# Optimization experiments

Hardware: AMD Instinct MI355X
Metric: run time of the kernel (lower is better)

Reference implementation:

```python
import jax, jax.numpy as jnp
import numpy as np

E = 2048   # embedding_size
H = 2048   # hidden_size
B = 512    # batch
OUT = 2    # output_size (coords)


def setup_inputs() -> dict:
    key = jax.random.key(0)
    ks = jax.random.split(key, 11)
    s = 0.02
    return {
        "embedding": jax.random.normal(ks[0], (B, E), dtype=jnp.float32),
        "max_seq_length": 256,
        "W_embed": jax.random.normal(ks[1], (H, E), dtype=jnp.float32) * s,
        "b_embed": jnp.zeros((H,), dtype=jnp.float32),
        "W_ih": jax.random.normal(ks[2], (4 * H, OUT), dtype=jnp.float32) * s,
        "b_ih": jnp.zeros((4 * H,), dtype=jnp.float32),
        "W_hh": jax.random.normal(ks[3], (4 * H, H), dtype=jnp.float32) * s,
        "b_hh": jnp.zeros((4 * H,), dtype=jnp.float32),
        "W_out": jax.random.normal(ks[4], (OUT, H), dtype=jnp.float32) * s,
        "b_out": jnp.zeros((OUT,), dtype=jnp.float32),
        "W_stop": jax.random.normal(ks[5], (1, H), dtype=jnp.float32) * s,
        "b_stop": jnp.zeros((1,), dtype=jnp.float32),
    }


def reference(embedding, max_seq_length, W_embed, b_embed, W_ih, b_ih,
              W_hh, b_hh, W_out, b_out, W_stop, b_stop):
    # h_0 from embedding head (num_layers == 1)
    h0 = embedding @ W_embed.T + b_embed          # (B, H)
    c0 = jnp.zeros_like(h0)
    x0 = jnp.zeros((embedding.shape[0], OUT), dtype=embedding.dtype)

    def step(carry, _):
        h, c, x = carry
        gates = x @ W_ih.T + b_ih + h @ W_hh.T + b_hh    # (B, 4H)
        i, f, g, o = jnp.split(gates, 4, axis=-1)         # torch gate order i,f,g,o
        c = jax.nn.sigmoid(f) * c + jax.nn.sigmoid(i) * jnp.tanh(g)
        h = jax.nn.sigmoid(o) * jnp.tanh(c)
        coord = h @ W_out.T + b_out                        # (B, 2)
        stop = jax.nn.sigmoid(h @ W_stop.T + b_stop)       # (B, 1)
        return (h, c, coord), (coord, stop)

    _, (coords, stops) = jax.lax.scan(step, (h0, c0, x0), xs=None,
                                      length=max_seq_length)
    outputs = jnp.transpose(coords, (1, 0, 2))     # (B, T, 2)
    stop_probs = jnp.transpose(stops, (1, 0, 2))   # (B, T, 1)
    return outputs, stop_probs
```

## Files before the change

kernel.cpp:

```cpp
#include <hip/hip_runtime.h>
#include <stdint.h>

#define E_DIM 2048
#define H_DIM 2048
#define B_DIM 512
#define T_DIM 256
#define G4H   8192

typedef unsigned short u16;
typedef __attribute__((ext_vector_type(8))) short bf16x8;
typedef __attribute__((ext_vector_type(4))) float f32x4;

__device__ inline u16 f2b(float f) {
  union { float f; uint32_t i; } v; v.f = f;
  uint32_t u = v.i;
  return (u16)((u + 0x7FFFu + ((u >> 16) & 1u)) >> 16);
}
__device__ inline float b2f(u16 u) {
  union { uint32_t i; float f; } v; v.i = ((uint32_t)u) << 16; return v.f;
}

__global__ __launch_bounds__(256) void convert_bf16(const float* __restrict__ s,
                                                    u16* __restrict__ d, int n4) {
  int i = blockIdx.x * 256 + threadIdx.x;
  if (i < n4) {
    float4 f = ((const float4*)s)[i];
    ushort4 o;
    o.x = f2b(f.x); o.y = f2b(f.y); o.z = f2b(f.z); o.w = f2b(f.w);
    ((ushort4*)d)[i] = o;
  }
}

__global__ __launch_bounds__(256) void build_weff(const float* __restrict__ W,
                                                  const float* __restrict__ W_ih,
                                                  const float* __restrict__ W_out,
                                                  u16* __restrict__ Wz) {
  int id = blockIdx.x * 256 + threadIdx.x;
  int lane = id & 63;
  int k32  = (id >> 6) & 63;
  int n16  = id >> 12;
  int np = n16 * 16 + (lane & 15);
  int k  = k32 * 32 + (lane >> 4) * 8;
  int g = np & 3, jrow = np >> 2;
  int src = g * H_DIM + jrow;
  float wi0 = W_ih[src * 2 + 0], wi1 = W_ih[src * 2 + 1];
  const float* sw = W + (size_t)src * H_DIM + k;
  u16 out[8];
  for (int j = 0; j < 8; ++j) {
    float v = sw[j] + wi0 * W_out[k + j] + wi1 * W_out[H_DIM + k + j];
    out[j] = f2b(v);
  }
  u16* dst = Wz + (size_t)id * 8;
  *(ushort4*)(dst) = *(ushort4*)&out[0];
  *(ushort4*)(dst + 4) = *(ushort4*)&out[4];
}

__global__ __launch_bounds__(256) void build_epi(const float* __restrict__ b_ih,
                                                 const float* __restrict__ b_hh,
                                                 const float* __restrict__ W_ih,
                                                 const float* __restrict__ b_out,
                                                 float* __restrict__ epi) {
  int np = blockIdx.x * 256 + threadIdx.x;
  int src = (np & 3) * H_DIM + (np >> 2);
  float wi0 = W_ih[src * 2 + 0], wi1 = W_ih[src * 2 + 1];
  float4 e;
  e.x = b_ih[src] + b_hh[src] + b_out[0] * wi0 + b_out[1] * wi1;
  e.y = wi0;
  e.z = wi1;
  e.w = 0.f;
  ((float4*)epi)[np] = e;
}

#define BM 64
#define BN 128
#define BK 32
__global__ __launch_bounds__(256) void gemm_bt(const u16* __restrict__ A,
                                               const u16* __restrict__ Bm,
                                               float* __restrict__ C,
                                               int M, int N, int K) {
  __shared__ u16 sA[BM * BK];
  __shared__ u16 sB[BN * BK];
  const int t = threadIdx.x;
  const int bm0 = blockIdx.y * BM, bn0 = blockIdx.x * BN;
  const int wave = t >> 6, lane = t & 63;
  const int wm = (wave >> 1) * 32, wn = (wave & 1) * 64;
  const int r16 = lane & 15, quad = lane >> 4;

  f32x4 acc[2][4];
  const f32x4 z = {0.f, 0.f, 0.f, 0.f};
  for (int i = 0; i < 2; ++i)
    for (int j = 0; j < 4; ++j) acc[i][j] = z;

  const int arow = t >> 2, acg = t & 3;

  for (int k0 = 0; k0 < K; k0 += BK) {
    __syncthreads();
    *(uint4*)&sA[arow * BK + acg * 8] =
        *(const uint4*)&A[(size_t)(bm0 + arow) * K + k0 + acg * 8];
    for (int i = 0; i < 2; ++i) {
      int c = t + 256 * i;
      int row = c >> 2, cg = c & 3;
      *(uint4*)&sB[row * BK + cg * 8] =
          *(const uint4*)&Bm[(size_t)(bn0 + row) * K + k0 + cg * 8];
    }
    __syncthreads();
    bf16x8 af[2], bfr[4];
    for (int mt = 0; mt < 2; ++mt)
      af[mt] = *(const bf16x8*)&sA[(wm + mt * 16 + r16) * BK + quad * 8];
    for (int nt = 0; nt < 4; ++nt)
      bfr[nt] = *(const bf16x8*)&sB[(wn + nt * 16 + r16) * BK + quad * 8];
    for (int mt = 0; mt < 2; ++mt)
      for (int nt = 0; nt < 4; ++nt)
        acc[mt][nt] = __builtin_amdgcn_mfma_f32_16x16x32_bf16(af[mt], bfr[nt],
                                                              acc[mt][nt], 0, 0, 0);
  }
  for (int mt = 0; mt < 2; ++mt)
    for (int nt = 0; nt < 4; ++nt) {
      int row = bm0 + wm + mt * 16 + quad * 4;
      int col = bn0 + wn + nt * 16 + r16;
      for (int r = 0; r < 4; ++r)
        C[(size_t)(row + r) * N + col] = acc[mt][nt][r];
    }
}

__global__ __launch_bounds__(256) void init_state(const float* __restrict__ h0pre,
                                                  const float* __restrict__ b_embed,
                                                  u16* __restrict__ h,
                                                  float* __restrict__ c,
                                                  float* __restrict__ xzero) {
  int idx = blockIdx.x * 256 + threadIdx.x;
  int bg = idx >> 11, k = idx & (H_DIM - 1);
  float v = h0pre[idx] + b_embed[k];
  size_t chunk = (((size_t)(bg >> 4)) * 64 + (k >> 5)) * 64 + ((k >> 3) & 3) * 16 + (bg & 15);
  size_t pos = chunk * 8 + (k & 7);
  h[pos] = f2b(v);
  c[pos] = 0.f;
  if (idx < B_DIM * 2) xzero[idx] = 0.f;
}

__global__ __launch_bounds__(64) void calc_xcorr(const float* __restrict__ h0pre,
                                                 const float* __restrict__ b_embed,
                                                 const float* __restrict__ W_out,
                                                 const float* __restrict__ b_out,
                                                 float* __restrict__ xc) {
  int m = blockIdx.x, ln = threadIdx.x;
  float s0 = 0.f, s1 = 0.f;
  for (int k = ln; k < H_DIM; k += 64) {
    float hv = h0pre[(size_t)m * H_DIM + k] + b_embed[k];
    s0 += hv * W_out[k];
    s1 += hv * W_out[H_DIM + k];
  }
  for (int off = 32; off > 0; off >>= 1) {
    s0 += __shfl_down(s0, off);
    s1 += __shfl_down(s1, off);
  }
  if (ln == 0) {
    xc[m * 2 + 0] = -(s0 + b_out[0]);
    xc[m * 2 + 1] = -(s1 + b_out[1]);
  }
}

__global__ __launch_bounds__(256) void init_out(const float* __restrict__ b_out,
                                                const float* __restrict__ b_stop,
                                                float* __restrict__ coords,
                                                float* __restrict__ stops) {
  int i = blockIdx.x * 256 + threadIdx.x;
  coords[i * 2 + 0] = b_out[0];
  coords[i * 2 + 1] = b_out[1];
  stops[i] = b_stop[0];
}

__global__ __launch_bounds__(256) void finalize_stops(float* __restrict__ stops) {
  int i = blockIdx.x * 256 + threadIdx.x;
  stops[i] = 1.f / (1.f + __expf(-stops[i]));
}

__global__ __launch_bounds__(512) void gemm_lstm(const u16* __restrict__ hA,
                                                 const u16* __restrict__ Wz,
                                                 const float* __restrict__ epi,
                                                 const float* __restrict__ x,
                                                 float* __restrict__ c,
                                                 u16* __restrict__ h_out,
                                                 const float* __restrict__ W_out,
                                                 const float* __restrict__ W_stop,
                                                 float* __restrict__ coords,
                                                 float* __restrict__ stops,
                                                 int trow) {
  __shared__ char smem[131072];
  float* cb = (float*)smem;
  float* gt = (float*)smem;

  const int bid = blockIdx.x;
  const int nt = (bid & 7) * 8 + ((bid >> 3) & 7);
  const int mt = bid >> 6;
  const int bm0 = mt * 128;

  const int t = threadIdx.x, wv = t >> 6, ln = t & 63;
  const int wn2 = wv & 1, kq = wv >> 1;
  const int r16 = ln & 15, quad = ln >> 4;

  const u16* pA[8];
  const u16* pB[4];
  for (int i = 0; i < 8; ++i)
    pA[i] = hA + (size_t)((bm0 >> 4) + i) * 32768 + (size_t)(kq * 16) * 512 + ln * 8;
  for (int i = 0; i < 4; ++i)
    pB[i] = Wz + (size_t)(nt * 8 + wn2 * 4 + i) * 32768 + (size_t)(kq * 16) * 512 + ln * 8;

  f32x4 acc[8][4];
  const f32x4 z = {0.f, 0.f, 0.f, 0.f};
  for (int i = 0; i < 8; ++i)
    for (int j = 0; j < 4; ++j) acc[i][j] = z;

  bf16x8 af[2][8], bf[2][4];
  for (int i = 0; i < 8; ++i) af[0][i] = *(const bf16x8*)(pA[i]);
  for (int i = 0; i < 4; ++i) bf[0][i] = *(const bf16x8*)(pB[i]);

#pragma unroll 2
  for (int kk = 0; kk < 16; ++kk) {
    const int cu = kk & 1;
    if (kk < 15) {
      const int nx = cu ^ 1;
      const size_t off = (size_t)(kk + 1) * 512;
      for (int i = 0; i < 8; ++i) af[nx][i] = *(const bf16x8*)(pA[i] + off);
      for (int i = 0; i < 4; ++i) bf[nx][i] = *(const bf16x8*)(pB[i] + off);
    }
    for (int mi = 0; mi < 8; ++mi)
      for (int ni = 0; ni < 4; ++ni)
        acc[mi][ni] = __builtin_amdgcn_mfma_f32_16x16x32_bf16(af[cu][mi], bf[cu][ni],
                                                              acc[mi][ni], 0, 0, 0);
  }

  if (kq >= 2) {
    float* dst = cb + ((kq - 2) * 2 + wn2) * 8192;
    for (int mi = 0; mi < 8; ++mi)
      for (int ni = 0; ni < 4; ++ni)
        *(f32x4*)&dst[((mi * 4 + ni) * 64 + ln) * 4] = acc[mi][ni];
  }
  __syncthreads();
  if (kq < 2) {
    const float* src = cb + (kq * 2 + wn2) * 8192;
    for (int mi = 0; mi < 8; ++mi)
      for (int ni = 0; ni < 4; ++ni)
        acc[mi][ni] += *(const f32x4*)&src[((mi * 4 + ni) * 64 + ln) * 4];
  }
  __syncthreads();
  if (kq == 1) {
    float* dst = cb + wn2 * 8192;
    for (int mi = 0; mi < 8; ++mi)
      for (int ni = 0; ni < 4; ++ni)
        *(f32x4*)&dst[((mi * 4 + ni) * 64 + ln) * 4] = acc[mi][ni];
  }
  __syncthreads();
  if (kq == 0) {
    const float* src = cb + wn2 * 8192;
    for (int mi = 0; mi < 8; ++mi)
      for (int ni = 0; ni < 4; ++ni)
        acc[mi][ni] += *(const f32x4*)&src[((mi * 4 + ni) * 64 + ln) * 4];
  }

  for (int half = 0; half < 2; ++half) {
    __syncthreads();
    if (wv < 2) {
      for (int mi = 0; mi < 4; ++mi)
        for (int ni = 0; ni < 4; ++ni) {
          int row = mi * 16 + quad * 4;
          int col = wn2 * 64 + ni * 16 + r16;
          f32x4 v = acc[half * 4 + mi][ni];
          for (int r = 0; r < 4; ++r)
            gt[(row + r) * 132 + col] = v[r];
        }
    }
    __syncthreads();
    if ((wv >> 2) == half) {
      const int q = wv & 3;
      const int lrow = q * 16 + r16;
      const int bg = bm0 + half * 64 + lrow;
      const float x0 = x[bg * 2 + 0], x1 = x[bg * 2 + 1];
      const size_t chunk = (((size_t)(bg >> 4)) * 64 + nt) * 64 + ln;
      const int hc0 = nt * 32 + quad * 8;
      float cv[8]; u16 hv[8];
      float s0 = 0.f, s1 = 0.f, s2 = 0.f;
      const float4* epi4 = (const float4*)epi;
      for (int j = 0; j < 8; ++j) {
        int col = quad * 32 + j * 4;
        float4 g4 = *(const float4*)&gt[lrow * 132 + col];
        float4 e0 = epi4[nt * 128 + col + 0];
        float4 e1 = epi4[nt * 128 + col + 1];
        float4 e2 = epi4[nt * 128 + col + 2];
        float4 e3 = epi4[nt * 128 + col + 3];
        float gi = g4.x + e0.x + x0 * e0.y + x1 * e0.z;
        float gf = g4.y + e1.x + x0 * e1.y + x1 * e1.z;
        float gg = g4.z + e2.x + x0 * e2.y + x1 * e2.z;
        float go = g4.w + e3.x + x0 * e3.y + x1 * e3.z;
        float si = 1.f / (1.f + __expf(-gi));
        float sf = 1.f / (1.f + __expf(-gf));
        float so = 1.f / (1.f + __expf(-go));
        float cn = sf * c[chunk * 8 + j] + si * tanhf(gg);
        cv[j] = cn;
        float hf = so * tanhf(cn);
        hv[j] = f2b(hf);
        s0 += hf * W_out[hc0 + j];
        s1 += hf * W_out[H_DIM + hc0 + j];
        s2 += hf * W_stop[hc0 + j];
      }
      *(float4*)&c[chunk * 8 + 0] = *(float4*)&cv[0];
      *(float4*)&c[chunk * 8 + 4] = *(float4*)&cv[4];
      *(ushort4*)&h_out[chunk * 8 + 0] = *(ushort4*)&hv[0];
      *(ushort4*)&h_out[chunk * 8 + 4] = *(ushort4*)&hv[4];
      s0 += __shfl_xor(s0, 16); s1 += __shfl_xor(s1, 16); s2 += __shfl_xor(s2, 16);
      s0 += __shfl_xor(s0, 32); s1 += __shfl_xor(s1, 32); s2 += __shfl_xor(s2, 32);
      if (quad == 0) {
        atomicAdd(&coords[((size_t)bg * T_DIM + trow) * 2 + 0], s0);
        atomicAdd(&coords[((size_t)bg * T_DIM + trow) * 2 + 1], s1);
        atomicAdd(&stops[(size_t)bg * T_DIM + trow], s2);
      }
    }
  }
}

extern "C" void kernel_launch(void* const* d_in, const int* in_sizes, int n_in,
                              void* d_out, int out_size, void* d_ws, size_t ws_size,
                              hipStream_t stream) {
  const float* embedding = (const float*)d_in[0];
  const float* W_embed   = (const float*)d_in[2];
  const float* b_embed   = (const float*)d_in[3];
  const float* W_ih      = (const float*)d_in[4];
  const float* b_ih      = (const float*)d_in[5];
  const float* W_hh      = (const float*)d_in[6];
  const float* b_hh      = (const float*)d_in[7];
  const float* W_out     = (const float*)d_in[8];
  const float* b_out     = (const float*)d_in[9];
  const float* W_stop    = (const float*)d_in[10];
  const float* b_stop    = (const float*)d_in[11];

  float* coords = (float*)d_out;
  float* stops  = (float*)d_out + (size_t)B_DIM * T_DIM * 2;

  char* ws = (char*)d_ws;
  u16* W_z     = (u16*)ws;   ws += (size_t)G4H * H_DIM * 2;
  u16* W_emb_b = (u16*)ws;   ws += (size_t)H_DIM * E_DIM * 2;
  u16* emb_b   = (u16*)ws;   ws += (size_t)B_DIM * E_DIM * 2;
  float* h0pre = (float*)ws; ws += (size_t)B_DIM * H_DIM * 4;
  float* epi   = (float*)ws; ws += (size_t)G4H * 4 * 4;
  float* cbuf  = (float*)ws; ws += (size_t)B_DIM * H_DIM * 4;
  u16* hbuf0   = (u16*)ws;   ws += (size_t)B_DIM * H_DIM * 2;
  u16* hbuf1   = (u16*)ws;   ws += (size_t)B_DIM * H_DIM * 2;
  float* xcorr = (float*)ws; ws += (size_t)B_DIM * 2 * 4;
  float* xzero = (float*)ws; ws += (size_t)B_DIM * 2 * 4;

  convert_bf16<<<(B_DIM * E_DIM / 4 + 255) / 256, 256, 0, stream>>>(embedding, emb_b, B_DIM * E_DIM / 4);
  convert_bf16<<<(H_DIM * E_DIM / 4 + 255) / 256, 256, 0, stream>>>(W_embed, W_emb_b, H_DIM * E_DIM / 4);
  build_weff<<<(G4H * H_DIM / 8) / 256, 256, 0, stream>>>(W_hh, W_ih, W_out, W_z);
  build_epi<<<G4H / 256, 256, 0, stream>>>(b_ih, b_hh, W_ih, b_out, epi);
  init_out<<<(B_DIM * T_DIM) / 256, 256, 0, stream>>>(b_out, b_stop, coords, stops);

  gemm_bt<<<dim3(H_DIM / BN, B_DIM / BM), 256, 0, stream>>>(emb_b, W_emb_b, h0pre,
                                                            B_DIM, H_DIM, E_DIM);
  init_state<<<(B_DIM * H_DIM) / 256, 256, 0, stream>>>(h0pre, b_embed, hbuf0, cbuf, xzero);
  calc_xcorr<<<B_DIM, 64, 0, stream>>>(h0pre, b_embed, W_out, b_out, xcorr);

  for (int t = 0; t < T_DIM; ++t) {
    u16* h_in  = (t & 1) ? hbuf1 : hbuf0;
    u16* h_out = (t & 1) ? hbuf0 : hbuf1;
    const float* xv = (t == 0) ? xcorr : xzero;
    gemm_lstm<<<256, 512, 0, stream>>>(h_in, W_z, epi, xv, cbuf, h_out,
                                       W_out, W_stop, coords, stops, t);
  }
  finalize_stops<<<(B_DIM * T_DIM) / 256, 256, 0, stream>>>(stops);
}
```

Baseline: 8.044 ms.

## Stage GEMM operand tiles into LDS via async global_load_lds with double buffering

Each step's LSTM GEMM previously had every wave load its A and B fragments straight from global memory into registers. Now the block cooperatively copies tiles into LDS with global_load_lds, double-buffered across K steps, and the waves then read fragments from LDS. The wave split changes from 4-way K partitioning to 2-way K by 2x2 M/N, which halves the per-wave accumulator and simplifies the cross-wave reduction and epilogue. The launch bounds now request 2 blocks per CU, but the 128KB LDS buffer may prevent that. A barrier is added on every K step.

```diff
diff --git a/kernel.cpp b/kernel.cpp
--- a/kernel.cpp
+++ b/kernel.cpp
@@ -18,6 +18,12 @@
 }
 __device__ inline float b2f(u16 u) {
   union { uint32_t i; float f; } v; v.i = ((uint32_t)u) << 16; return v.f;
+}
+
+__device__ __forceinline__ void stage16(const void* g, void* l) {
+  __builtin_amdgcn_global_load_lds(
+      (const __attribute__((address_space(1))) uint32_t*)g,
+      (__attribute__((address_space(3))) uint32_t*)l, 16, 0, 0);
 }
 
 __global__ __launch_bounds__(256) void convert_bf16(const float* __restrict__ s,
@@ -175,7 +181,7 @@
   stops[i] = 1.f / (1.f + __expf(-stops[i]));
 }
 
-__global__ __launch_bounds__(512) void gemm_lstm(const u16* __restrict__ hA,
+__global__ __launch_bounds__(512, 2) void gemm_lstm(const u16* __restrict__ hA,
                                                  const u16* __restrict__ Wz,
                                                  const float* __restrict__ epi,
                                                  const float* __restrict__ x,
@@ -186,9 +192,7 @@
                                                  float* __restrict__ coords,
                                                  float* __restrict__ stops,
                                                  int trow) {
-  __shared__ char smem[131072];
-  float* cb = (float*)smem;
-  float* gt = (float*)smem;
+  __shared__ __align__(16) char smem[131072];
 
   const int bid = blockIdx.x;
   const int nt = (bid & 7) * 8 + ((bid >> 3) & 7);
@@ -196,124 +200,150 @@
   const int bm0 = mt * 128;
 
   const int t = threadIdx.x, wv = t >> 6, ln = t & 63;
-  const int wn2 = wv & 1, kq = wv >> 1;
+  const int kq = wv >> 2, wm = (wv >> 1) & 1, wn = wv & 1;
   const int r16 = ln & 15, quad = ln >> 4;
 
-  const u16* pA[8];
-  const u16* pB[4];
-  for (int i = 0; i < 8; ++i)
-    pA[i] = hA + (size_t)((bm0 >> 4) + i) * 32768 + (size_t)(kq * 16) * 512 + ln * 8;
+  const u16* gptr[8];
+  uint32_t ldsoff[8];
+#pragma unroll
+  for (int s = 0; s < 8; ++s) {
+    int ti = wv * 8 + s;
+    int g = ti >> 4;
+    int w = ti & 15;
+    int rowi = w >> 1, kc2 = w & 1;
+    int kqg = g >> 1, isB = g & 1;
+    int kc = kqg * 32 + kc2;
+    if (isB)
+      gptr[s] = Wz + ((size_t)(nt * 8 + rowi) * 64 + kc) * 512 + ln * 8;
+    else
+      gptr[s] = hA + ((size_t)((bm0 >> 4) + rowi) * 64 + kc) * 512 + ln * 8;
+    ldsoff[s] = (uint32_t)(kqg * 65536 + isB * 16384 + w * 1024);
+  }
+
+#pragma unroll
+  for (int s = 0; s < 8; ++s) stage16(gptr[s], smem + ldsoff[s]);
+#pragma unroll
+  for (int s = 0; s < 8; ++s) gptr[s] += 1024;
+  __syncthreads();
+
+  f32x4 acc[4][4];
+  const f32x4 z = {0.f, 0.f, 0.f, 0.f};
+#pragma unroll
   for (int i = 0; i < 4; ++i)
-    pB[i] = Wz + (size_t)(nt * 8 + wn2 * 4 + i) * 32768 + (size_t)(kq * 16) * 512 + ln * 8;
-
-  f32x4 acc[8][4];
-  const f32x4 z = {0.f, 0.f, 0.f, 0.f};
-  for (int i = 0; i < 8; ++i)
+#pragma unroll
     for (int j = 0; j < 4; ++j) acc[i][j] = z;
 
-  bf16x8 af[2][8], bf[2][4];
-  for (int i = 0; i < 8; ++i) af[0][i] = *(const bf16x8*)(pA[i]);
-  for (int i = 0; i < 4; ++i) bf[0][i] = *(const bf16x8*)(pB[i]);
-
-#pragma unroll 2
-  for (int kk = 0; kk < 16; ++kk) {
-    const int cu = kk & 1;
-    if (kk < 15) {
-      const int nx = cu ^ 1;
-      const size_t off = (size_t)(kk + 1) * 512;
-      for (int i = 0; i < 8; ++i) af[nx][i] = *(const bf16x8*)(pA[i] + off);
-      for (int i = 0; i < 4; ++i) bf[nx][i] = *(const bf16x8*)(pB[i] + off);
-    }
-    for (int mi = 0; mi < 8; ++mi)
-      for (int ni = 0; ni < 4; ++ni)
-        acc[mi][ni] = __builtin_amdgcn_mfma_f32_16x16x32_bf16(af[cu][mi], bf[cu][ni],
-                                                              acc[mi][ni], 0, 0, 0);
-  }
-
-  if (kq >= 2) {
-    float* dst = cb + ((kq - 2) * 2 + wn2) * 8192;
-    for (int mi = 0; mi < 8; ++mi)
+  const uint32_t rdbase0 = (uint32_t)(kq * 65536);
+
+  for (int p = 0; p < 16; ++p) {
+    if (p < 15) {
+      const uint32_t tog = (uint32_t)(((p + 1) & 1) * 32768);
+#pragma unroll
+      for (int s = 0; s < 8; ++s) stage16(gptr[s], smem + (ldsoff[s] + tog));
+#pragma unroll
+      for (int s = 0; s < 8; ++s) gptr[s] += 1024;
+    }
+    const char* rb = smem + rdbase0 + (uint32_t)((p & 1) * 32768);
+#pragma unroll
+    for (int kc2 = 0; kc2 < 2; ++kc2) {
+      bf16x8 af[4], bf[4];
+#pragma unroll
+      for (int i = 0; i < 4; ++i)
+        af[i] = *(const bf16x8*)(rb + ((wm * 4 + i) * 2 + kc2) * 1024 + ln * 16);
+#pragma unroll
+      for (int i = 0; i < 4; ++i)
+        bf[i] = *(const bf16x8*)(rb + 16384 + ((wn * 4 + i) * 2 + kc2) * 1024 + ln * 16);
+#pragma unroll
+      for (int mi = 0; mi < 4; ++mi)
+#pragma unroll
+        for (int ni = 0; ni < 4; ++ni)
+          acc[mi][ni] = __builtin_amdgcn_mfma_f32_16x16x32_bf16(af[mi], bf[ni],
+                                                                acc[mi][ni], 0, 0, 0);
+    }
+    __syncthreads();
+  }
+
+  float* cb = (float*)smem;
+  if (kq == 1) {
+    float* dst = cb + (wm * 2 + wn) * 4096;
+#pragma unroll
+    for (int mi = 0; mi < 4; ++mi)
+#pragma unroll
       for (int ni = 0; ni < 4; ++ni)
         *(f32x4*)&dst[((mi * 4 + ni) * 64 + ln) * 4] = acc[mi][ni];
   }
   __syncthreads();
-  if (kq < 2) {
-    const float* src = cb + (kq * 2 + wn2) * 8192;
-    for (int mi = 0; mi < 8; ++mi)
+  if (kq == 0) {
+    const float* src = cb + (wm * 2 + wn) * 4096;
+#pragma unroll
+    for (int mi = 0; mi < 4; ++mi)
+#pragma unroll
       for (int ni = 0; ni < 4; ++ni)
         acc[mi][ni] += *(const f32x4*)&src[((mi * 4 + ni) * 64 + ln) * 4];
   }
   __syncthreads();
-  if (kq == 1) {
-    float* dst = cb + wn2 * 8192;
-    for (int mi = 0; mi < 8; ++mi)
-      for (int ni = 0; ni < 4; ++ni)
-        *(f32x4*)&dst[((mi * 4 + ni) * 64 + ln) * 4] = acc[mi][ni];
+
+  float* gt = (float*)smem;
+  if (kq == 0) {
+#pragma unroll
+    for (int mi = 0; mi < 4; ++mi)
+#pragma unroll
+      for (int ni = 0; ni < 4; ++ni) {
+        int row = wm * 64 + mi * 16 + quad * 4;
+        int col = wn * 64 + ni * 16 + r16;
+        f32x4 v = acc[mi][ni];
+#pragma unroll
+        for (int r = 0; r < 4; ++r)
+          gt[(row + r) * 132 + col] = v[r];
+      }
   }
   __syncthreads();
-  if (kq == 0) {
-    const float* src = cb + wn2 * 8192;
-    for (int mi = 0; mi < 8; ++mi)
-      for (int ni = 0; ni < 4; ++ni)
-        acc[mi][ni] += *(const f32x4*)&src[((mi * 4 + ni) * 64 + ln) * 4];
-  }
-
-  for (int half = 0; half < 2; ++half) {
-    __syncthreads();
-    if (wv < 2) {
-      for (int mi = 0; mi < 4; ++mi)
-        for (int ni = 0; ni < 4; ++ni) {
-          int row = mi * 16 + quad * 4;
-          int col = wn2 * 64 + ni * 16 + r16;
-          f32x4 v = acc[half * 4 + mi][ni];
-          for (int r = 0; r < 4; ++r)
-            gt[(row + r) * 132 + col] = v[r];
-        }
-    }
-    __syncthreads();
-    if ((wv >> 2) == half) {
-      const int q = wv & 3;
-      const int lrow = q * 16 + r16;
-      const int bg = bm0 + half * 64 + lrow;
-      const float x0 = x[bg * 2 + 0], x1 = x[bg * 2 + 1];
-      const size_t chunk = (((size_t)(bg >> 4)) * 64 + nt) * 64 + ln;
-      const int hc0 = nt * 32 + quad * 8;
-      float cv[8]; u16 hv[8];
-      float s0 = 0.f, s1 = 0.f, s2 = 0.f;
-      const float4* epi4 = (const float4*)epi;
-      for (int j = 0; j < 8; ++j) {
-        int col = quad * 32 + j * 4;
-        float4 g4 = *(const float4*)&gt[lrow * 132 + col];
-        float4 e0 = epi4[nt * 128 + col + 0];
-        float4 e1 = epi4[nt * 128 + col + 1];
-        float4 e2 = epi4[nt * 128 + col + 2];
-        float4 e3 = epi4[nt * 128 + col + 3];
-        float gi = g4.x + e0.x + x0 * e0.y + x1 * e0.z;
-        float gf = g4.y + e1.x + x0 * e1.y + x1 * e1.z;
-        float gg = g4.z + e2.x + x0 * e2.y + x1 * e2.z;
-        float go = g4.w + e3.x + x0 * e3.y + x1 * e3.z;
-        float si = 1.f / (1.f + __expf(-gi));
-        float sf = 1.f / (1.f + __expf(-gf));
-        float so = 1.f / (1.f + __expf(-go));
-        float cn = sf * c[chunk * 8 + j] + si * tanhf(gg);
-        cv[j] = cn;
-        float hf = so * tanhf(cn);
-        hv[j] = f2b(hf);
-        s0 += hf * W_out[hc0 + j];
-        s1 += hf * W_out[H_DIM + hc0 + j];
-        s2 += hf * W_stop[hc0 + j];
-      }
-      *(float4*)&c[chunk * 8 + 0] = *(float4*)&cv[0];
-      *(float4*)&c[chunk * 8 + 4] = *(float4*)&cv[4];
-      *(ushort4*)&h_out[chunk * 8 + 0] = *(ushort4*)&hv[0];
-      *(ushort4*)&h_out[chunk * 8 + 4] = *(ushort4*)&hv[4];
-      s0 += __shfl_xor(s0, 16); s1 += __shfl_xor(s1, 16); s2 += __shfl_xor(s2, 16);
-      s0 += __shfl_xor(s0, 32); s1 += __shfl_xor(s1, 32); s2 += __shfl_xor(s2, 32);
-      if (quad == 0) {
-        atomicAdd(&coords[((size_t)bg * T_DIM + trow) * 2 + 0], s0);
-        atomicAdd(&coords[((size_t)bg * T_DIM + trow) * 2 + 1], s1);
-        atomicAdd(&stops[(size_t)bg * T_DIM + trow], s2);
-      }
+
+  {
+    const int lrow = wv * 16 + r16;
+    const int bg = bm0 + lrow;
+    const float x0 = x[bg * 2 + 0], x1 = x[bg * 2 + 1];
+    const size_t chunk = (((size_t)(bg >> 4)) * 64 + nt) * 64 + ln;
+    const int hc0 = nt * 32 + quad * 8;
+    float cv[8]; u16 hv[8];
+    float s0 = 0.f, s1 = 0.f, s2 = 0.f;
+    const float4* epi4 = (const float4*)epi;
+    f32x4 cold0 = *(const f32x4*)&c[chunk * 8 + 0];
+    f32x4 cold1 = *(const f32x4*)&c[chunk * 8 + 4];
+#pragma unroll
+    for (int j = 0; j < 8; ++j) {
+      int col = quad * 32 + j * 4;
+      float4 g4 = *(const float4*)&gt[lrow * 132 + col];
+      float4 e0 = epi4[nt * 128 + col + 0];
+      float4 e1 = epi4[nt * 128 + col + 1];
+      float4 e2 = epi4[nt * 128 + col + 2];
+      float4 e3 = epi4[nt * 128 + col + 3];
+      float gi = g4.x + e0.x + x0 * e0.y + x1 * e0.z;
+      float gf = g4.y + e1.x + x0 * e1.y + x1 * e1.z;
+      float gg = g4.z + e2.x + x0 * e2.y + x1 * e2.z;
+      float go = g4.w + e3.x + x0 * e3.y + x1 * e3.z;
+      float si = 1.f / (1.f + __expf(-gi));
+      float sf = 1.f / (1.f + __expf(-gf));
+      float so = 1.f / (1.f + __expf(-go));
+      float cold = (j < 4) ? cold0[j & 3] : cold1[j & 3];
+      float cn = sf * cold + si * tanhf(gg);
+      cv[j] = cn;
+      float hf = so * tanhf(cn);
+      hv[j] = f2b(hf);
+      s0 += hf * W_out[hc0 + j];
+      s1 += hf * W_out[H_DIM + hc0 + j];
+      s2 += hf * W_stop[hc0 + j];
+    }
+    *(float4*)&c[chunk * 8 + 0] = *(float4*)&cv[0];
+    *(float4*)&c[chunk * 8 + 4] = *(float4*)&cv[4];
+    *(ushort4*)&h_out[chunk * 8 + 0] = *(ushort4*)&hv[0];
+    *(ushort4*)&h_out[chunk * 8 + 4] = *(ushort4*)&hv[4];
+    s0 += __shfl_xor(s0, 16); s1 += __shfl_xor(s1, 16); s2 += __shfl_xor(s2, 16);
+    s0 += __shfl_xor(s0, 32); s1 += __shfl_xor(s1, 32); s2 += __shfl_xor(s2, 32);
+    if (quad == 0) {
+      atomicAdd(&coords[((size_t)bg * T_DIM + trow) * 2 + 0], s0);
+      atomicAdd(&coords[((size_t)bg * T_DIM + trow) * 2 + 1], s1);
+      atomicAdd(&stops[(size_t)bg * T_DIM + trow], s2);
     }
   }
 }
```

New measurement: 7.217 ms. 10.3% less time.
